# Kernel optimization log

Measured on AMD Instinct MI355X. Metric: run time of the kernel, lower is better.

The kernel has to match this reference:

```python
import jax, jax.numpy as jnp
import numpy as np

B, LIN, E, D, N = 32, 2048, 512, 512, 2  # batch, enc len, enc hidden, dec hidden, dec layers


def setup_inputs() -> dict:
    key = jax.random.key(0)
    k1, k2, k3, k4, k5 = jax.random.split(key, 5)
    d_hidden = jax.random.normal(k1, (B, N, D), dtype=jnp.float32)
    encoder_outputs = jax.random.normal(k2, (B, LIN, E), dtype=jnp.float32)
    fan_in = E + N * D
    lim1 = 1.0 / np.sqrt(fan_in)
    W1 = jax.random.uniform(k3, (fan_in, D), minval=-lim1, maxval=lim1, dtype=jnp.float32)
    b1 = jax.random.uniform(k4, (D,), minval=-lim1, maxval=lim1, dtype=jnp.float32)
    lim2 = 1.0 / np.sqrt(D)
    w2 = jax.random.uniform(k5, (D,), minval=-lim2, maxval=lim2, dtype=jnp.float32)
    return {"d_hidden": d_hidden, "encoder_outputs": encoder_outputs,
            "W1": W1, "b1": b1, "w2": w2}


def reference(d_hidden, encoder_outputs, W1, b1, w2):
    # Faithful to: tanh(Linear(cat(repeat(d_hidden), enc))) -> Linear(.,1) -> softmax
    # cat@W1 == d_flat@W1_d + enc@W1_e (broadcast-add avoids materializing the concat).
    nd = d_hidden.shape[1] * d_hidden.shape[2]
    d_flat = d_hidden.reshape(d_hidden.shape[0], nd)        # [B, N*D]
    W1_d, W1_e = W1[:nd], W1[nd:]                            # [N*D,D], [E,D]
    dec_proj = d_flat @ W1_d + b1                            # [B, D]
    enc_proj = jnp.einsum('ble,ed->bld', encoder_outputs, W1_e)  # [B, Lin, D]
    attn_hidden = jnp.tanh(enc_proj + dec_proj[:, None, :])  # [B, Lin, D]
    scores = jnp.einsum('bld,d->bl', attn_hidden, w2)        # [B, Lin]
    return jax.nn.softmax(scores, axis=-1)
```

## Files before the change

### kernel.cpp

```cpp
#include <hip/hip_runtime.h>
#include <hip/hip_bf16.h>

#define L_SZ 2048
#define E_SZ 512
#define D_SZ 512
#define ND   1024
#define WS_DEC_OFF 0
#define WS_BT_OFF  (32*512*4)
#define WS_SC_OFF  (32*512*4 + 512*512*2)

typedef unsigned short ushort_t;
typedef unsigned int   uint_t;
typedef __attribute__((ext_vector_type(8))) short short8;
typedef __attribute__((ext_vector_type(4))) float floatx4;
typedef __attribute__((ext_vector_type(4))) float fvec4;

__device__ __forceinline__ ushort_t f2bf(float f) {
  uint_t u = __builtin_bit_cast(uint_t, f);
  u += 0x7fffu + ((u >> 16) & 1u);
  return (ushort_t)(u >> 16);
}

__device__ __forceinline__ float fast_tanh(float x) {
  float e = __expf(2.0f * x);
  return 1.0f - 2.0f * __builtin_amdgcn_rcpf(e + 1.0f);
}

__device__ __forceinline__ void dma16(const ushort_t* g, ushort_t* l) {
  __builtin_amdgcn_global_load_lds(
      (const __attribute__((address_space(1))) uint_t*)(const void*)g,
      (__attribute__((address_space(3))) uint_t*)(void*)l,
      16, 0, 0);
}

__global__ __launch_bounds__(256) void prep_k(const float* __restrict__ dh,
                                              const float* __restrict__ W1,
                                              const float* __restrict__ b1,
                                              float* __restrict__ dec,
                                              ushort_t* __restrict__ Bt) {
  int blk = blockIdx.x, t = threadIdx.x;
  if (blk < 256) {
    int b = blk >> 3, d = (blk & 7) * 64 + (t & 63);
    int q = t >> 6;
    __shared__ float red[4][64];
    const float* dfb = dh + b * ND;
    float s = 0.f;
    #pragma unroll 8
    for (int k = q * 256; k < q * 256 + 256; k++)
      s = fmaf(dfb[k], W1[k * D_SZ + d], s);
    red[q][t & 63] = s;
    __syncthreads();
    if (q == 0)
      dec[b * D_SZ + d] = red[0][t] + red[1][t] + red[2][t] + red[3][t] + b1[d];
  } else {
    int tid = blk - 256;
    int tk = (tid >> 4) * 32, tn = (tid & 15) * 32;
    __shared__ float tile[32][33];
    int cc = t & 31, r8 = t >> 5;
    #pragma unroll
    for (int p = 0; p < 4; p++) {
      int r = r8 + p * 8;
      tile[r][cc] = W1[(ND + tk + r) * D_SZ + tn + cc];
    }
    __syncthreads();
    #pragma unroll
    for (int p = 0; p < 4; p++) {
      int nn = r8 + p * 8;
      Bt[(tn + nn) * E_SZ + tk + cc] = f2bf(tile[cc][nn]);
    }
  }
}

__global__ __launch_bounds__(512, 2) void main_k(const float* __restrict__ enc,
                                                 const ushort_t* __restrict__ Bt,
                                                 const float* __restrict__ dec,
                                                 const float* __restrict__ w2,
                                                 float* __restrict__ scores) {
  const int b  = blockIdx.y;
  const int l0 = blockIdx.x * 64;
  const int t  = threadIdx.x;
  const int wave = t >> 6, lane = t & 63;
  const int col = lane & 15, quad = lane >> 4;

  __shared__ __align__(16) ushort_t Bs[2][512 * 64];
  __shared__ __align__(16) ushort_t As[2][64 * 64];
  __shared__ float s_sc[64];

  if (t < 64) s_sc[t] = 0.f;

  floatx4 acc[4][4];
  #pragma unroll
  for (int mt = 0; mt < 4; mt++)
    #pragma unroll
    for (int nt = 0; nt < 4; nt++)
      acc[mt][nt] = (floatx4){0.f, 0.f, 0.f, 0.f};

  const float* arow = enc + (size_t)(b * L_SZ + l0) * E_SZ;

  const int am = t >> 3, ac = t & 7;
  const float* aptr = arow + am * E_SZ + ac * 8;
  const int awoff = am * 64 + ((ac ^ (am & 7)) << 3);

  const int bn0 = wave * 64 + (lane >> 3);
  const int bc0 = (lane & 7) ^ ((lane >> 3) & 7);
  const ushort_t* bptr0 = Bt + bn0 * E_SZ + bc0 * 8;

  fvec4 ra0 = *(const fvec4*)aptr;
  fvec4 ra1 = *(const fvec4*)(aptr + 4);
  #pragma unroll
  for (int j = 0; j < 8; j++)
    dma16(bptr0 + j * 8 * E_SZ, &Bs[0][wave * 4096 + j * 512]);
  fvec4 rn0 = *(const fvec4*)(aptr + 64);
  fvec4 rn1 = *(const fvec4*)(aptr + 68);
  asm volatile("s_waitcnt vmcnt(10)" ::: "memory");
  {
    union { short8 v; __hip_bfloat162 h[4]; } pk;
    pk.h[0] = __float22bfloat162_rn(make_float2(ra0.x, ra0.y));
    pk.h[1] = __float22bfloat162_rn(make_float2(ra0.z, ra0.w));
    pk.h[2] = __float22bfloat162_rn(make_float2(ra1.x, ra1.y));
    pk.h[3] = __float22bfloat162_rn(make_float2(ra1.z, ra1.w));
    *(short8*)&As[0][awoff] = pk.v;
  }
  ra0 = rn0; ra1 = rn1;
  asm volatile("s_waitcnt lgkmcnt(0)" ::: "memory");
  __builtin_amdgcn_s_barrier();
  __builtin_amdgcn_sched_barrier(0);

  #pragma unroll 1
  for (int kw = 0; kw < 8; kw++) {
    const ushort_t* Acur = &As[kw & 1][0];
    const ushort_t* Bcur = &Bs[kw & 1][0];

    if (kw < 6) {
      const float* ap = aptr + (kw + 2) * 64;
      rn0 = *(const fvec4*)ap;
      rn1 = *(const fvec4*)(ap + 4);
    }
    if (kw < 7) {
      const ushort_t* bp = bptr0 + (kw + 1) * 64;
      ushort_t* bld = &Bs[(kw + 1) & 1][wave * 4096];
      #pragma unroll
      for (int j = 0; j < 8; j++)
        dma16(bp + j * 8 * E_SZ, bld + j * 512);
    }

    if (kw < 6)      asm volatile("s_waitcnt vmcnt(10)" ::: "memory");
    else if (kw == 6) asm volatile("s_waitcnt vmcnt(8)"  ::: "memory");
    else              asm volatile("s_waitcnt vmcnt(0)"  ::: "memory");

    if (kw < 7) {
      union { short8 v; __hip_bfloat162 h[4]; } pk;
      pk.h[0] = __float22bfloat162_rn(make_float2(ra0.x, ra0.y));
      pk.h[1] = __float22bfloat162_rn(make_float2(ra0.z, ra0.w));
      pk.h[2] = __float22bfloat162_rn(make_float2(ra1.x, ra1.y));
      pk.h[3] = __float22bfloat162_rn(make_float2(ra1.z, ra1.w));
      *(short8*)&As[(kw + 1) & 1][awoff] = pk.v;
      ra0 = rn0; ra1 = rn1;
    }

    #pragma unroll
    for (int ks = 0; ks < 2; ks++) {
      short8 af[4], bfr[4];
      #pragma unroll
      for (int mt = 0; mt < 4; mt++) {
        int m = mt * 16 + col;
        af[mt] = *(const short8*)&Acur[m * 64 + ((((ks << 2) + quad) ^ (m & 7)) << 3)];
      }
      #pragma unroll
      for (int nt = 0; nt < 4; nt++) {
        int n = wave * 64 + nt * 16 + col;
        bfr[nt] = *(const short8*)&Bcur[n * 64 + ((((ks << 2) + quad) ^ (n & 7)) << 3)];
      }
      #pragma unroll
      for (int mt = 0; mt < 4; mt++)
        #pragma unroll
        for (int nt = 0; nt < 4; nt++)
          acc[mt][nt] = __builtin_amdgcn_mfma_f32_16x16x32_bf16(af[mt], bfr[nt], acc[mt][nt], 0, 0, 0);
    }

    asm volatile("s_waitcnt lgkmcnt(0)" ::: "memory");
    __builtin_amdgcn_s_barrier();
    __builtin_amdgcn_sched_barrier(0);
  }

  const float* decb = dec + b * D_SZ;
  float sums[4][4];
  #pragma unroll
  for (int mt = 0; mt < 4; mt++)
    #pragma unroll
    for (int r = 0; r < 4; r++) sums[mt][r] = 0.f;

  #pragma unroll
  for (int nt = 0; nt < 4; nt++) {
    int n = wave * 64 + nt * 16 + col;
    float dv = decb[n];
    float wv = w2[n];
    #pragma unroll
    for (int mt = 0; mt < 4; mt++)
      #pragma unroll
      for (int r = 0; r < 4; r++)
        sums[mt][r] += fast_tanh(acc[mt][nt][r] + dv) * wv;
  }
  #pragma unroll
  for (int mt = 0; mt < 4; mt++) {
    #pragma unroll
    for (int r = 0; r < 4; r++) {
      float v = sums[mt][r];
      v += __shfl_xor(v, 1, 16);
      v += __shfl_xor(v, 2, 16);
      v += __shfl_xor(v, 4, 16);
      v += __shfl_xor(v, 8, 16);
      if (col == 0) atomicAdd(&s_sc[mt * 16 + quad * 4 + r], v);
    }
  }
  __syncthreads();
  if (t < 64) scores[b * L_SZ + l0 + t] = s_sc[t];
}

__global__ __launch_bounds__(1024) void softmax_k(const float* __restrict__ sc,
                                                  float* __restrict__ out) {
  int b = blockIdx.x, t = threadIdx.x;
  int wave = t >> 6, lane = t & 63;
  __shared__ float redm[16], reds[16];
  const float* row = sc + b * L_SZ;
  float v0 = row[t], v1 = row[t + 1024];
  float mx = fmaxf(v0, v1);
  #pragma unroll
  for (int off = 32; off >= 1; off >>= 1) mx = fmaxf(mx, __shfl_xor(mx, off, 64));
  if (lane == 0) redm[wave] = mx;
  __syncthreads();
  float m = redm[0];
  #pragma unroll
  for (int i = 1; i < 16; i++) m = fmaxf(m, redm[i]);
  v0 = __expf(v0 - m);
  v1 = __expf(v1 - m);
  float s = v0 + v1;
  #pragma unroll
  for (int off = 32; off >= 1; off >>= 1) s += __shfl_xor(s, off, 64);
  if (lane == 0) reds[wave] = s;
  __syncthreads();
  float sum = reds[0];
  #pragma unroll
  for (int i = 1; i < 16; i++) sum += reds[i];
  float inv = 1.0f / sum;
  out[b * L_SZ + t]        = v0 * inv;
  out[b * L_SZ + t + 1024] = v1 * inv;
}

extern "C" void kernel_launch(void* const* d_in, const int* in_sizes, int n_in,
                              void* d_out, int out_size, void* d_ws, size_t ws_size,
                              hipStream_t stream) {
  const float* d_hidden = (const float*)d_in[0];
  const float* enc      = (const float*)d_in[1];
  const float* W1       = (const float*)d_in[2];
  const float* b1       = (const float*)d_in[3];
  const float* w2       = (const float*)d_in[4];
  float* out = (float*)d_out;

  char* ws = (char*)d_ws;
  float*    dec = (float*)(ws + WS_DEC_OFF);
  ushort_t* Bt  = (ushort_t*)(ws + WS_BT_OFF);
  float*    sc  = (float*)(ws + WS_SC_OFF);

  prep_k<<<512, 256, 0, stream>>>(d_hidden, W1, b1, dec, Bt);
  main_k<<<dim3(32, 32), 512, 0, stream>>>(enc, Bt, dec, w2, sc);
  softmax_k<<<32, 1024, 0, stream>>>(sc, out);
}
```

Baseline: 259.3 us.

## Double main kernel M tile to 128 rows and single-buffer the A tile

Each block now handles 128 encoder rows instead of 64, which halves the number of times the shared bf16 weight tile is reloaded from global memory. The grid shrinks to 16x32 blocks. The A tile moves from a double buffer to a single buffer, with an extra barrier per k-step so the conversion and store happen after compute. This doubles the accumulator registers (acc[8][4]), which may lower occupancy below two blocks per CU, and leaves only 512 blocks for the machine.

```diff
diff --git a/kernel.cpp b/kernel.cpp
--- a/kernel.cpp
+++ b/kernel.cpp
@@ -77,64 +77,76 @@
                                                  const float* __restrict__ w2,
                                                  float* __restrict__ scores) {
   const int b  = blockIdx.y;
-  const int l0 = blockIdx.x * 64;
+  const int l0 = blockIdx.x * 128;
   const int t  = threadIdx.x;
   const int wave = t >> 6, lane = t & 63;
   const int col = lane & 15, quad = lane >> 4;
 
   __shared__ __align__(16) ushort_t Bs[2][512 * 64];
-  __shared__ __align__(16) ushort_t As[2][64 * 64];
-  __shared__ float s_sc[64];
-
-  if (t < 64) s_sc[t] = 0.f;
-
-  floatx4 acc[4][4];
-  #pragma unroll
-  for (int mt = 0; mt < 4; mt++)
+  __shared__ __align__(16) ushort_t As[128 * 64];
+  __shared__ float s_sc[128];
+
+  if (t < 128) s_sc[t] = 0.f;
+
+  floatx4 acc[8][4];
+  #pragma unroll
+  for (int mt = 0; mt < 8; mt++)
     #pragma unroll
     for (int nt = 0; nt < 4; nt++)
       acc[mt][nt] = (floatx4){0.f, 0.f, 0.f, 0.f};
 
   const float* arow = enc + (size_t)(b * L_SZ + l0) * E_SZ;
 
-  const int am = t >> 3, ac = t & 7;
-  const float* aptr = arow + am * E_SZ + ac * 8;
-  const int awoff = am * 64 + ((ac ^ (am & 7)) << 3);
+  const int am = t >> 2, ac0 = (t & 3) * 2;
+  const float* aptr = arow + am * E_SZ + ac0 * 8;
+  const int awoff0 = am * 64 + ((ac0 ^ (am & 7)) << 3);
+  const int awoff1 = am * 64 + (((ac0 + 1) ^ (am & 7)) << 3);
 
   const int bn0 = wave * 64 + (lane >> 3);
   const int bc0 = (lane & 7) ^ ((lane >> 3) & 7);
   const ushort_t* bptr0 = Bt + bn0 * E_SZ + bc0 * 8;
 
-  fvec4 ra0 = *(const fvec4*)aptr;
-  fvec4 ra1 = *(const fvec4*)(aptr + 4);
+  fvec4 a00 = *(const fvec4*)aptr;
+  fvec4 a01 = *(const fvec4*)(aptr + 4);
+  fvec4 a02 = *(const fvec4*)(aptr + 8);
+  fvec4 a03 = *(const fvec4*)(aptr + 12);
   #pragma unroll
   for (int j = 0; j < 8; j++)
     dma16(bptr0 + j * 8 * E_SZ, &Bs[0][wave * 4096 + j * 512]);
-  fvec4 rn0 = *(const fvec4*)(aptr + 64);
-  fvec4 rn1 = *(const fvec4*)(aptr + 68);
-  asm volatile("s_waitcnt vmcnt(10)" ::: "memory");
+  fvec4 ra0 = *(const fvec4*)(aptr + 64);
+  fvec4 ra1 = *(const fvec4*)(aptr + 68);
+  fvec4 ra2 = *(const fvec4*)(aptr + 72);
+  fvec4 ra3 = *(const fvec4*)(aptr + 76);
+  asm volatile("s_waitcnt vmcnt(12)" ::: "memory");
   {
-    union { short8 v; __hip_bfloat162 h[4]; } pk;
-    pk.h[0] = __float22bfloat162_rn(make_float2(ra0.x, ra0.y));
-    pk.h[1] = __float22bfloat162_rn(make_float2(ra0.z, ra0.w));
-    pk.h[2] = __float22bfloat162_rn(make_float2(ra1.x, ra1.y));
-    pk.h[3] = __float22bfloat162_rn(make_float2(ra1.z, ra1.w));
-    *(short8*)&As[0][awoff] = pk.v;
-  }
-  ra0 = rn0; ra1 = rn1;
+    union { short8 v; __hip_bfloat162 h[4]; } p0, p1;
+    p0.h[0] = __float22bfloat162_rn(make_float2(a00.x, a00.y));
+    p0.h[1] = __float22bfloat162_rn(make_float2(a00.z, a00.w));
+    p0.h[2] = __float22bfloat162_rn(make_float2(a01.x, a01.y));
+    p0.h[3] = __float22bfloat162_rn(make_float2(a01.z, a01.w));
+    p1.h[0] = __float22bfloat162_rn(make_float2(a02.x, a02.y));
+    p1.h[1] = __float22bfloat162_rn(make_float2(a02.z, a02.w));
+    p1.h[2] = __float22bfloat162_rn(make_float2(a03.x, a03.y));
+    p1.h[3] = __float22bfloat162_rn(make_float2(a03.z, a03.w));
+    *(short8*)&As[awoff0] = p0.v;
+    *(short8*)&As[awoff1] = p1.v;
+  }
   asm volatile("s_waitcnt lgkmcnt(0)" ::: "memory");
   __builtin_amdgcn_s_barrier();
   __builtin_amdgcn_sched_barrier(0);
 
+  fvec4 rn0, rn1, rn2, rn3;
+
   #pragma unroll 1
   for (int kw = 0; kw < 8; kw++) {
-    const ushort_t* Acur = &As[kw & 1][0];
     const ushort_t* Bcur = &Bs[kw & 1][0];
 
     if (kw < 6) {
       const float* ap = aptr + (kw + 2) * 64;
       rn0 = *(const fvec4*)ap;
       rn1 = *(const fvec4*)(ap + 4);
+      rn2 = *(const fvec4*)(ap + 8);
+      rn3 = *(const fvec4*)(ap + 12);
     }
     if (kw < 7) {
       const ushort_t* bp = bptr0 + (kw + 1) * 64;
@@ -144,27 +156,17 @@
         dma16(bp + j * 8 * E_SZ, bld + j * 512);
     }
 
-    if (kw < 6)      asm volatile("s_waitcnt vmcnt(10)" ::: "memory");
+    if (kw < 6)       asm volatile("s_waitcnt vmcnt(12)" ::: "memory");
     else if (kw == 6) asm volatile("s_waitcnt vmcnt(8)"  ::: "memory");
     else              asm volatile("s_waitcnt vmcnt(0)"  ::: "memory");
 
-    if (kw < 7) {
-      union { short8 v; __hip_bfloat162 h[4]; } pk;
-      pk.h[0] = __float22bfloat162_rn(make_float2(ra0.x, ra0.y));
-      pk.h[1] = __float22bfloat162_rn(make_float2(ra0.z, ra0.w));
-      pk.h[2] = __float22bfloat162_rn(make_float2(ra1.x, ra1.y));
-      pk.h[3] = __float22bfloat162_rn(make_float2(ra1.z, ra1.w));
-      *(short8*)&As[(kw + 1) & 1][awoff] = pk.v;
-      ra0 = rn0; ra1 = rn1;
-    }
-
     #pragma unroll
     for (int ks = 0; ks < 2; ks++) {
-      short8 af[4], bfr[4];
-      #pragma unroll
-      for (int mt = 0; mt < 4; mt++) {
+      short8 af[8], bfr[4];
+      #pragma unroll
+      for (int mt = 0; mt < 8; mt++) {
         int m = mt * 16 + col;
-        af[mt] = *(const short8*)&Acur[m * 64 + ((((ks << 2) + quad) ^ (m & 7)) << 3)];
+        af[mt] = *(const short8*)&As[m * 64 + ((((ks << 2) + quad) ^ (m & 7)) << 3)];
       }
       #pragma unroll
       for (int nt = 0; nt < 4; nt++) {
@@ -172,7 +174,7 @@
         bfr[nt] = *(const short8*)&Bcur[n * 64 + ((((ks << 2) + quad) ^ (n & 7)) << 3)];
       }
       #pragma unroll
-      for (int mt = 0; mt < 4; mt++)
+      for (int mt = 0; mt < 8; mt++)
         #pragma unroll
         for (int nt = 0; nt < 4; nt++)
           acc[mt][nt] = __builtin_amdgcn_mfma_f32_16x16x32_bf16(af[mt], bfr[nt], acc[mt][nt], 0, 0, 0);
@@ -180,13 +182,30 @@
 
     asm volatile("s_waitcnt lgkmcnt(0)" ::: "memory");
     __builtin_amdgcn_s_barrier();
+
+    if (kw < 7) {
+      union { short8 v; __hip_bfloat162 h[4]; } p0, p1;
+      p0.h[0] = __float22bfloat162_rn(make_float2(ra0.x, ra0.y));
+      p0.h[1] = __float22bfloat162_rn(make_float2(ra0.z, ra0.w));
+      p0.h[2] = __float22bfloat162_rn(make_float2(ra1.x, ra1.y));
+      p0.h[3] = __float22bfloat162_rn(make_float2(ra1.z, ra1.w));
+      p1.h[0] = __float22bfloat162_rn(make_float2(ra2.x, ra2.y));
+      p1.h[1] = __float22bfloat162_rn(make_float2(ra2.z, ra2.w));
+      p1.h[2] = __float22bfloat162_rn(make_float2(ra3.x, ra3.y));
+      p1.h[3] = __float22bfloat162_rn(make_float2(ra3.z, ra3.w));
+      *(short8*)&As[awoff0] = p0.v;
+      *(short8*)&As[awoff1] = p1.v;
+      ra0 = rn0; ra1 = rn1; ra2 = rn2; ra3 = rn3;
+    }
+    asm volatile("s_waitcnt lgkmcnt(0)" ::: "memory");
+    __builtin_amdgcn_s_barrier();
     __builtin_amdgcn_sched_barrier(0);
   }
 
   const float* decb = dec + b * D_SZ;
-  float sums[4][4];
-  #pragma unroll
-  for (int mt = 0; mt < 4; mt++)
+  float sums[8][4];
+  #pragma unroll
+  for (int mt = 0; mt < 8; mt++)
     #pragma unroll
     for (int r = 0; r < 4; r++) sums[mt][r] = 0.f;
 
@@ -196,13 +215,13 @@
     float dv = decb[n];
     float wv = w2[n];
     #pragma unroll
-    for (int mt = 0; mt < 4; mt++)
+    for (int mt = 0; mt < 8; mt++)
       #pragma unroll
       for (int r = 0; r < 4; r++)
         sums[mt][r] += fast_tanh(acc[mt][nt][r] + dv) * wv;
   }
   #pragma unroll
-  for (int mt = 0; mt < 4; mt++) {
+  for (int mt = 0; mt < 8; mt++) {
     #pragma unroll
     for (int r = 0; r < 4; r++) {
       float v = sums[mt][r];
@@ -214,7 +233,7 @@
     }
   }
   __syncthreads();
-  if (t < 64) scores[b * L_SZ + l0 + t] = s_sc[t];
+  if (t < 128) scores[b * L_SZ + l0 + t] = s_sc[t];
 }
 
 __global__ __launch_bounds__(1024) void softmax_k(const float* __restrict__ sc,
@@ -263,6 +282,6 @@
   float*    sc  = (float*)(ws + WS_SC_OFF);
 
   prep_k<<<512, 256, 0, stream>>>(d_hidden, W1, b1, dec, Bt);
-  main_k<<<dim3(32, 32), 512, 0, stream>>>(enc, Bt, dec, w2, sc);
+  main_k<<<dim3(16, 32), 512, 0, stream>>>(enc, Bt, dec, w2, sc);
   softmax_k<<<32, 1024, 0, stream>>>(sc, out);
 }
```

New measurement: 249.3 us. 1.04x faster.
